# Kernel optimization log

Measured on AMD Instinct MI355X. Metric: run time of the kernel, lower is better.

Reference implementation:

```python
import jax, jax.numpy as jnp
import numpy as np

FFT_NORM = "forward"


def _deq_cplx(qp, scale, mn):
    # qp stores (q_int8 + 127) in [0, 254]; dequant: qp*scale + min, last dim = (re, im)
    f = qp.astype(jnp.float32) * scale + mn
    return jax.lax.complex(f[..., 0], f[..., 1])


def setup_inputs() -> dict:
    key = jax.random.key(0)
    ks = jax.random.split(key, 16)
    B, Cin, Cout, H, W = 8, 32, 32, 256, 256
    NxW, NyW = 32, 17            # half-modes of the spectral weight
    r0, r1, r2, r3 = 16, 16, 16, 9  # Tucker ranks
    inp = {
        "x": jax.random.normal(ks[0], (B, Cin, H, W), dtype=jnp.float32),
        "core_scale": jax.random.uniform(ks[1], (), jnp.float32, 0.001, 0.02),
        "core_min": jax.random.normal(ks[2], (), jnp.float32) * 0.1,
        "factor_scales": jax.random.uniform(ks[3], (4,), jnp.float32, 0.001, 0.02),
        "factor_mins": jax.random.normal(ks[4], (4,), jnp.float32) * 0.1,
        "b_scale": jax.random.uniform(ks[5], (), jnp.float32, 0.001, 0.02),
        "b_min": jax.random.normal(ks[6], (), jnp.float32) * 0.1,
        "q_core": jax.random.randint(ks[7], (r0, r1, r2, r3, 2), 0, 255, jnp.int32),
        "q_f0": jax.random.randint(ks[8], (Cin, r0, 2), 0, 255, jnp.int32),
        "q_f1": jax.random.randint(ks[9], (Cout, r1, 2), 0, 255, jnp.int32),
        "q_f2": jax.random.randint(ks[10], (NxW, r2, 2), 0, 255, jnp.int32),
        "q_f3": jax.random.randint(ks[11], (NyW, r3, 2), 0, 255, jnp.int32),
        "q_bias": jax.random.randint(ks[12], (Cout,), 0, 255, jnp.int32),
    }
    return inp


def reference(x, core_scale, core_min, factor_scales, factor_mins, b_scale, b_min,
              q_core, q_f0, q_f1, q_f2, q_f3, q_bias):
    # 1) rFFT over the last two (spatial) dims
    x_fft = jnp.fft.rfftn(x, axes=(-2, -1), norm=FFT_NORM)  # [B, Cin, Nx, Ny_r] c64

    # 2) dequantize Tucker core + factors, reconstruct complex weight via multi_mode_dot
    core = _deq_cplx(q_core, core_scale, core_min)                       # [r0,r1,r2,r3]
    F0 = _deq_cplx(q_f0, factor_scales[0], factor_mins[0])               # [Cin, r0]
    F1 = _deq_cplx(q_f1, factor_scales[1], factor_mins[1])               # [Cout, r1]
    F2 = _deq_cplx(q_f2, factor_scales[2], factor_mins[2])               # [NxW, r2]
    F3 = _deq_cplx(q_f3, factor_scales[3], factor_mins[3])               # [NyW, r3]
    W = jnp.einsum('ijkl,ai,bj,ck,dl->abcd', core, F0, F1, F2, F3)       # [Cin,Cout,NxW,NyW]

    B, Cin, Nx, Ny_r = x_fft.shape
    CinW, Cout, NxW, NyW = W.shape
    assert Cin == CinW

    # 3) centered-slice channel mixing (faithful to the original double loop)
    cx, nx_neg, nx_pos = Nx // 2, NxW // 2, NxW // 2 + NxW % 2
    cy, ny_neg, ny_pos = Ny_r // 2, NyW // 2, NyW // 2 + NyW % 2
    sx = slice(cx - nx_neg, cx + nx_pos)
    sy = slice(cy - ny_neg, cy + ny_pos)
    Wx = slice(0, nx_pos + nx_neg)
    Wy = slice(0, ny_pos + ny_neg)

    mixed = jnp.einsum('bixy,ioxy->boxy', x_fft[:, :, sx, sy], W[:, :, Wx, Wy])
    out_fft = jnp.zeros((B, Cout, Nx, Ny_r), dtype=x_fft.dtype).at[:, :, sx, sy].set(mixed)

    # 4) inverse rFFT back to the original spatial size
    x_out = jnp.fft.irfftn(out_fft, s=x.shape[2:], axes=(-2, -1), norm=FFT_NORM)

    # 5) dequantized bias (real)
    bias = q_bias.astype(jnp.float32) * b_scale + b_min
    return x_out + bias[None, :, None, None]
```

## Files before the change

### kernel.cpp

```cpp
#include <hip/hip_runtime.h>


__device__ __forceinline__ float2 cfma(float2 a, float2 b, float2 c) {
    c.x = fmaf(a.x, b.x, fmaf(-a.y, b.y, c.x));
    c.y = fmaf(a.x, b.y, fmaf(a.y, b.x, c.y));
    return c;
}
__device__ __forceinline__ float2 cmul(float2 a, float2 b) {
    return make_float2(a.x*b.x - a.y*b.y, a.x*b.y + a.y*b.x);
}

__global__ __launch_bounds__(256) void wprep_kernel(
    const int* __restrict__ q_core, const int* __restrict__ q_f3,
    const float* __restrict__ core_scale, const float* __restrict__ core_min,
    const float* __restrict__ f_scales, const float* __restrict__ f_mins,
    float2* __restrict__ CL)
{
    int d = blockIdx.x >> 4, k = blockIdx.x & 15;
    int ij = threadIdx.x;
    float cs = *core_scale, cm = *core_min;
    float s3 = f_scales[3], m3 = f_mins[3];
    const int* qc = q_core + ((ij*16 + k)*9)*2;
    float2 acc = make_float2(0.f, 0.f);
#pragma unroll
    for (int l = 0; l < 9; ++l) {
        int2 q = *(const int2*)(qc + l*2);
        float2 ce = make_float2(q.x*cs + cm, q.y*cs + cm);
        float2 f3 = make_float2(q_f3[(d*9+l)*2]*s3 + m3, q_f3[(d*9+l)*2+1]*s3 + m3);
        acc = cfma(ce, f3, acc);
    }
    CL[(d*16 + k)*256 + ij] = acc;
}

__global__ __launch_bounds__(256) void weights_kernel(
    const float2* __restrict__ CL, const int* __restrict__ q_f0,
    const int* __restrict__ q_f1, const int* __restrict__ q_f2,
    const float* __restrict__ f_scales, const float* __restrict__ f_mins,
    float2* __restrict__ W4)
{
    __shared__ float2 F0s[512], F1s[512];
    __shared__ float2 C2p[16*17];
    __shared__ float2 A2p[16*33];
    int t = threadIdx.x, m = blockIdx.x;
    int c = m / 17, d = m % 17;
    float s0 = f_scales[0], m0 = f_mins[0];
    float s1 = f_scales[1], m1 = f_mins[1];
    float s2 = f_scales[2], m2 = f_mins[2];

    for (int e = t; e < 512; e += 256) {
        F0s[e] = make_float2(q_f0[2*e]*s0 + m0, q_f0[2*e+1]*s0 + m0);
        F1s[e] = make_float2(q_f1[2*e]*s1 + m1, q_f1[2*e+1]*s1 + m1);
    }
    {
        float2 acc = make_float2(0.f, 0.f);
#pragma unroll
        for (int k = 0; k < 16; ++k) {
            float2 clv = CL[(d*16 + k)*256 + t];
            float2 f2 = make_float2(q_f2[(c*16+k)*2]*s2 + m2,
                                    q_f2[(c*16+k)*2+1]*s2 + m2);
            acc = cfma(clv, f2, acc);
        }
        __syncthreads();
        C2p[(t >> 4)*17 + (t & 15)] = acc;
    }
    __syncthreads();
#pragma unroll
    for (int r = 0; r < 2; ++r) {
        int e = t + r*256; int i = e & 15, b = e >> 4;
        float2 acc = make_float2(0.f, 0.f);
#pragma unroll
        for (int j = 0; j < 16; ++j)
            acc = cfma(C2p[i*17 + j], F1s[b*16 + j], acc);
        A2p[i*33 + b] = acc;
    }
    __syncthreads();
    {
        int b = t & 31, a0 = t >> 5;
#pragma unroll
        for (int q = 0; q < 4; ++q) {
            int a = a0 + 8*q;
            float2 acc = make_float2(0.f, 0.f);
#pragma unroll
            for (int i = 0; i < 16; ++i)
                acc = cfma(F0s[a*16 + i], A2p[i*33 + b], acc);
            W4[m*1024 + a*32 + b] = acc;
        }
    }
}

template<int P>
__device__ __forceinline__ void quad_acc(float& ar, float& ai, float xv, float tx, float ty) {
    if (P == 0) { ar = fmaf(xv, tx, ar);  ai = fmaf(xv, ty, ai); }
    if (P == 1) { ar = fmaf(xv, ty, ar);  ai = fmaf(-xv, tx, ai); }
    if (P == 2) { ar = fmaf(-xv, tx, ar); ai = fmaf(-xv, ty, ai); }
    if (P == 3) { ar = fmaf(-xv, ty, ar); ai = fmaf(xv, tx, ai); }
}

template<int KY0, int NKY>
__device__ __forceinline__ void fwdw_body(int lane, int row0, const float* xs,
                                          float2* __restrict__ A1)
{
    float ar[NKY], ai[NKY], tr[NKY], ti[NKY], sr[NKY], si[NKY];
#pragma unroll
    for (int j = 0; j < NKY; ++j) {
        ar[j] = 0.f; ai[j] = 0.f;
        const int kk = KY0 + j + 56;
        float a = kk * (1.f/128.f);
        sr[j] = cospif(a); si[j] = -sinpif(a);
        tr[j] = 1.f; ti[j] = 0.f;
    }
    for (int w = 0; w < 64; ++w) {
        float xv0 = xs[w*65 + lane];
        float xv1 = xs[(w+64)*65 + lane];
        float xv2 = xs[(w+128)*65 + lane];
        float xv3 = xs[(w+192)*65 + lane];
#pragma unroll
        for (int j = 0; j < NKY; ++j) {
            float tx = tr[j], ty = ti[j];
            const int pj = (KY0 + 56 + j) & 3;
            switch (pj) {
                case 0:
                    quad_acc<0>(ar[j], ai[j], xv0, tx, ty);
                    quad_acc<0>(ar[j], ai[j], xv1, tx, ty);
                    quad_acc<0>(ar[j], ai[j], xv2, tx, ty);
                    quad_acc<0>(ar[j], ai[j], xv3, tx, ty);
                    break;
                case 1:
                    quad_acc<0>(ar[j], ai[j], xv0, tx, ty);
                    quad_acc<1>(ar[j], ai[j], xv1, tx, ty);
                    quad_acc<2>(ar[j], ai[j], xv2, tx, ty);
                    quad_acc<3>(ar[j], ai[j], xv3, tx, ty);
                    break;
                case 2:
                    quad_acc<0>(ar[j], ai[j], xv0, tx, ty);
                    quad_acc<2>(ar[j], ai[j], xv1, tx, ty);
                    quad_acc<0>(ar[j], ai[j], xv2, tx, ty);
                    quad_acc<2>(ar[j], ai[j], xv3, tx, ty);
                    break;
                default:
                    quad_acc<0>(ar[j], ai[j], xv0, tx, ty);
                    quad_acc<3>(ar[j], ai[j], xv1, tx, ty);
                    quad_acc<2>(ar[j], ai[j], xv2, tx, ty);
                    quad_acc<1>(ar[j], ai[j], xv3, tx, ty);
                    break;
            }
            tr[j] = fmaf(tx, sr[j], -ty*si[j]);
            ti[j] = fmaf(tx, si[j],  ty*sr[j]);
        }
    }
    int row = row0 + lane;
#pragma unroll
    for (int j = 0; j < NKY; ++j)
        A1[(KY0 + j)*65536 + row] = make_float2(ar[j], ai[j]);
}

__global__ __launch_bounds__(256) void fwd_w_kernel(const float* __restrict__ x,
                                                    float2* __restrict__ A1)
{
    __shared__ float xs[256*65];
    int tid = threadIdx.x;
    int row0 = blockIdx.x * 64;
    const float2* xf2 = (const float2*)x;
    for (int i2 = tid; i2 < 8192; i2 += 256) {
        int r = i2 >> 7, w2 = i2 & 127;
        float2 v = xf2[(size_t)(row0 + r)*128 + w2];
        xs[(2*w2)*65 + r]   = v.x;
        xs[(2*w2+1)*65 + r] = v.y;
    }
    __syncthreads();
    int lane = tid & 63, g = tid >> 6;
    if      (g == 0) fwdw_body<0, 5>(lane, row0, xs, A1);
    else if (g == 1) fwdw_body<5, 4>(lane, row0, xs, A1);
    else if (g == 2) fwdw_body<9, 4>(lane, row0, xs, A1);
    else             fwdw_body<13,4>(lane, row0, xs, A1);
}

__global__ __launch_bounds__(256) void fwd_h_kernel(const float2* __restrict__ A1,
                                                    float2* __restrict__ X)
{
    __shared__ float2 tbl[256];
    __shared__ float as_re[8*264];
    __shared__ float as_im[8*264];
    int tid = threadIdx.x;
    int ky = blockIdx.x >> 5, bi0 = (blockIdx.x & 31) * 8;
    tbl[tid] = make_float2(cospif(tid * (1.f/128.f)), -sinpif(tid * (1.f/128.f)));
    for (int idx = tid; idx < 2048; idx += 256) {
        int b = idx >> 8, h = idx & 255;
        float2 v = A1[ky*65536 + (bi0 + b)*256 + h];
        int ad = (h >> 5)*264 + (h & 31)*8 + b;
        as_re[ad] = v.x; as_im[ad] = v.y;
    }
    __syncthreads();
    int lane = tid & 63, g = tid >> 6;
    int bl = lane & 7, q = lane >> 3;
    int kx0 = g * 8;
    float2 acc[8];
#pragma unroll
    for (int j = 0; j < 8; ++j) acc[j] = make_float2(0.f, 0.f);
    int base = q*264 + bl;
    for (int hh = 0; hh < 32; ++hh) {
        float ar = as_re[base + hh*8];
        float ai = as_im[base + hh*8];
#pragma unroll
        for (int j = 0; j < 8; ++j) {
            int kk = kx0 + j + 112;
            float2 t = tbl[(kk * hh) & 255];
            acc[j].x = fmaf(ar, t.x, fmaf(-ai, t.y, acc[j].x));
            acc[j].y = fmaf(ar, t.y, fmaf( ai, t.x, acc[j].y));
        }
    }
    float2 fstep = tbl[q * 32];
    float2 f = make_float2(1.f, 0.f);
#pragma unroll
    for (int j = 0; j < 8; ++j) {
        float2 v = cmul(acc[j], f);
        v.x += __shfl_xor(v.x, 8);  v.y += __shfl_xor(v.y, 8);
        v.x += __shfl_xor(v.x, 16); v.y += __shfl_xor(v.y, 16);
        v.x += __shfl_xor(v.x, 32); v.y += __shfl_xor(v.y, 32);
        acc[j] = v;
        f = cmul(f, fstep);
    }
    if (q == 0) {
        const float inv = 1.f / 65536.f;
#pragma unroll
        for (int j = 0; j < 8; ++j)
            X[((kx0 + j)*17 + ky)*256 + bi0 + bl] =
                make_float2(acc[j].x * inv, acc[j].y * inv);
    }
}

__global__ __launch_bounds__(256) void mix_kernel(const float2* __restrict__ X,
                                                  const float2* __restrict__ W4,
                                                  float2* __restrict__ Mx)
{
    __shared__ float2 Xs[256];
    __shared__ float2 Ws[1024];
    int tid = threadIdx.x, mode = blockIdx.x;
    Xs[tid] = X[mode*256 + tid];
    for (int idx = tid; idx < 1024; idx += 256) Ws[idx] = W4[mode*1024 + idx];
    __syncthreads();
    int b = tid >> 5, o = tid & 31;
    float2 acc = make_float2(0.f, 0.f);
#pragma unroll
    for (int i = 0; i < 32; ++i)
        acc = cfma(Xs[b*32 + i], Ws[i*32 + o], acc);
    Mx[mode*256 + tid] = acc;
}

template<int KY0, int NK>
__device__ __forceinline__ void invh_part(int h, int hh, const float2* ms, float2* Ts)
{
    float2 acc[NK];
#pragma unroll
    for (int j = 0; j < NK; ++j) acc[j] = make_float2(0.f, 0.f);
    int n0 = (112 * h) & 255;
    float tr = cospif(n0 * (1.f/128.f)), ti = sinpif(n0 * (1.f/128.f));
    float sr = cospif(h  * (1.f/128.f)), si = sinpif(h  * (1.f/128.f));
    for (int kx = 0; kx < 32; ++kx) {
#pragma unroll
        for (int j = 0; j < NK; ++j) {
            float2 mv = ms[kx*17 + KY0 + j];
            acc[j].x = fmaf(mv.x, tr, fmaf(-mv.y, ti, acc[j].x));
            acc[j].y = fmaf(mv.x, ti, fmaf( mv.y, tr, acc[j].y));
        }
        float ntr = fmaf(tr, sr, -ti*si);
        ti = fmaf(tr, si, ti*sr);
        tr = ntr;
    }
#pragma unroll
    for (int j = 0; j < NK; ++j) Ts[hh*18 + KY0 + j] = acc[j];
}

__global__ __launch_bounds__(256) void inv_kernel(const float2* __restrict__ Mx,
                                                  const int* __restrict__ q_bias,
                                                  const float* __restrict__ b_scale,
                                                  const float* __restrict__ b_min,
                                                  float* __restrict__ out)
{
    __shared__ float2 ms[544];
    __shared__ __align__(16) float2 Ts[32*18];
    int tid = threadIdx.x;
    int bo = blockIdx.x & 255, hc = blockIdx.x >> 8;
    for (int idx = tid; idx < 544; idx += 256) ms[idx] = Mx[idx*256 + bo];
    __syncthreads();
    {
        int hh = tid & 31, g = tid >> 5;
        int h = hc*32 + hh;
        if (g < 7) {
            switch (g) {
                case 0: invh_part<0, 2>(h, hh, ms, Ts); break;
                case 1: invh_part<2, 2>(h, hh, ms, Ts); break;
                case 2: invh_part<4, 2>(h, hh, ms, Ts); break;
                case 3: invh_part<6, 2>(h, hh, ms, Ts); break;
                case 4: invh_part<8, 2>(h, hh, ms, Ts); break;
                case 5: invh_part<10,2>(h, hh, ms, Ts); break;
                default:invh_part<12,2>(h, hh, ms, Ts); break;
            }
        } else {
            invh_part<14,3>(h, hh, ms, Ts);
        }
    }
    __syncthreads();
    {
        int w0 = tid & 63, hs = tid >> 6;
        float C[17], S[17];
        {
            int n0 = (56 * w0) & 255;
            float tr = cospif(n0 * (1.f/128.f)), ti = sinpif(n0 * (1.f/128.f));
            float sr = cospif(w0 * (1.f/128.f)), si = sinpif(w0 * (1.f/128.f));
#pragma unroll
            for (int ky = 0; ky < 17; ++ky) {
                C[ky] = tr; S[ky] = ti;
                float ntr = fmaf(tr, sr, -ti*si);
                ti = fmaf(tr, si, ti*sr);
                tr = ntr;
            }
        }
        float bias = q_bias[bo & 31] * (*b_scale) + (*b_min);
        float* obase = out + (size_t)bo*65536 + (size_t)hc*32*256;

#pragma unroll
        for (int r = 0; r < 8; ++r) {
            int hh = hs*8 + r;
            const float4* tp = (const float4*)&Ts[hh*18];
            float R0 = 0.f, R1 = 0.f, R2 = 0.f, R3 = 0.f, I1 = 0.f, I3 = 0.f;
#pragma unroll
            for (int kp = 0; kp < 9; ++kp) {
                float vx0, vy0, vx1 = 0.f, vy1 = 0.f;
                if (kp < 8) {
                    float4 v4 = tp[kp];
                    vx0 = v4.x; vy0 = v4.y; vx1 = v4.z; vy1 = v4.w;
                } else {
                    float2 v2 = Ts[hh*18 + 16];
                    vx0 = v2.x; vy0 = v2.y;
                }
#pragma unroll
                for (int half = 0; half < 2; ++half) {
                    if (kp == 8 && half == 1) break;
                    const int ky = 2*kp + half;
                    float vx = half ? vx1 : vx0;
                    float vy = half ? vy1 : vy0;
                    float ur = fmaf(vx, C[ky], -vy*S[ky]);
                    if ((ky & 1) == 0) {
                        if ((ky & 3) == 0) R0 += ur; else R2 += ur;
                    } else {
                        float ui = fmaf(vx, S[ky], vy*C[ky]);
                        if ((ky & 3) == 1) { R1 += ur; I1 += ui; }
                        else               { R3 += ur; I3 += ui; }
                    }
                }
            }
            float e02 = R0 + R2, d02 = R0 - R2;
            float e13 = R1 + R3, di  = I3 - I1;
            float q0 = e02 + e13, q2 = e02 - e13;
            float q1 = d02 + di,  q3 = d02 - di;
            obase[hh*256 + w0]       = fmaf(2.f, q0, bias);
            obase[hh*256 + w0 + 64]  = fmaf(2.f, q1, bias);
            obase[hh*256 + w0 + 128] = fmaf(2.f, q2, bias);
            obase[hh*256 + w0 + 192] = fmaf(2.f, q3, bias);
        }
    }
}

extern "C" void kernel_launch(void* const* d_in, const int* in_sizes, int n_in,
                              void* d_out, int out_size, void* d_ws, size_t ws_size,
                              hipStream_t stream) {
    const float* x          = (const float*)d_in[0];
    const float* core_scale = (const float*)d_in[1];
    const float* core_min   = (const float*)d_in[2];
    const float* f_scales   = (const float*)d_in[3];
    const float* f_mins     = (const float*)d_in[4];
    const float* b_scale    = (const float*)d_in[5];
    const float* b_min      = (const float*)d_in[6];
    const int* q_core = (const int*)d_in[7];
    const int* q_f0   = (const int*)d_in[8];
    const int* q_f1   = (const int*)d_in[9];
    const int* q_f2   = (const int*)d_in[10];
    const int* q_f3   = (const int*)d_in[11];
    const int* q_bias = (const int*)d_in[12];
    float* out = (float*)d_out;

    float2* ws = (float2*)d_ws;
    float2* A1 = ws;
    float2* W4 = ws + 1114112;
    float2* X  = W4 + 557056;
    float2* Mx = X + 139264;
    float2* CL = Mx + 139264;
    (void)ws_size; (void)n_in; (void)in_sizes; (void)out_size;

    wprep_kernel<<<272, 256, 0, stream>>>(q_core, q_f3, core_scale, core_min,
                                          f_scales, f_mins, CL);
    weights_kernel<<<544, 256, 0, stream>>>(CL, q_f0, q_f1, q_f2,
                                            f_scales, f_mins, W4);
    fwd_w_kernel<<<1024, 256, 0, stream>>>(x, A1);
    fwd_h_kernel<<<544, 256, 0, stream>>>(A1, X);
    mix_kernel<<<544, 256, 0, stream>>>(X, W4, Mx);
    inv_kernel<<<2048, 256, 0, stream>>>(Mx, q_bias, b_scale, b_min, out);
}
```

Measured before the change: 199.8 us.

## Split width DFT by frequency residue mod 4 with precomputed twiddle table

The width-direction partial DFT now folds the four quarter-length input segments with butterflies at load time (sums and differences), so each frequency class (k mod 4 = 0, 1, 2, 3) is computed from 64 combined samples instead of 256. The twiddles come from a shared-memory table indexed by (k*w) mod 256 rather than being advanced by a recurrence. This cuts the inner-loop FMA count roughly in half and removes drift from the twiddle recurrence. In exchange it adds shared-memory table reads and puts a different per-group workload on each wave (group 0 handles 5 frequencies, the others handle 4).

```diff
diff --git a/kernel.cpp b/kernel.cpp
--- a/kernel.cpp
+++ b/kernel.cpp
@@ -88,91 +88,90 @@
     }
 }
 
-template<int P>
-__device__ __forceinline__ void quad_acc(float& ar, float& ai, float xv, float tx, float ty) {
-    if (P == 0) { ar = fmaf(xv, tx, ar);  ai = fmaf(xv, ty, ai); }
-    if (P == 1) { ar = fmaf(xv, ty, ar);  ai = fmaf(-xv, tx, ai); }
-    if (P == 2) { ar = fmaf(-xv, tx, ar); ai = fmaf(-xv, ty, ai); }
-    if (P == 3) { ar = fmaf(-xv, ty, ar); ai = fmaf(xv, tx, ai); }
-}
-
-template<int KY0, int NKY>
-__device__ __forceinline__ void fwdw_body(int lane, int row0, const float* xs,
-                                          float2* __restrict__ A1)
-{
-    float ar[NKY], ai[NKY], tr[NKY], ti[NKY], sr[NKY], si[NKY];
-#pragma unroll
-    for (int j = 0; j < NKY; ++j) {
-        ar[j] = 0.f; ai[j] = 0.f;
-        const int kk = KY0 + j + 56;
-        float a = kk * (1.f/128.f);
-        sr[j] = cospif(a); si[j] = -sinpif(a);
-        tr[j] = 1.f; ti[j] = 0.f;
-    }
-    for (int w = 0; w < 64; ++w) {
-        float xv0 = xs[w*65 + lane];
-        float xv1 = xs[(w+64)*65 + lane];
-        float xv2 = xs[(w+128)*65 + lane];
-        float xv3 = xs[(w+192)*65 + lane];
-#pragma unroll
-        for (int j = 0; j < NKY; ++j) {
-            float tx = tr[j], ty = ti[j];
-            const int pj = (KY0 + 56 + j) & 3;
-            switch (pj) {
-                case 0:
-                    quad_acc<0>(ar[j], ai[j], xv0, tx, ty);
-                    quad_acc<0>(ar[j], ai[j], xv1, tx, ty);
-                    quad_acc<0>(ar[j], ai[j], xv2, tx, ty);
-                    quad_acc<0>(ar[j], ai[j], xv3, tx, ty);
-                    break;
-                case 1:
-                    quad_acc<0>(ar[j], ai[j], xv0, tx, ty);
-                    quad_acc<1>(ar[j], ai[j], xv1, tx, ty);
-                    quad_acc<2>(ar[j], ai[j], xv2, tx, ty);
-                    quad_acc<3>(ar[j], ai[j], xv3, tx, ty);
-                    break;
-                case 2:
-                    quad_acc<0>(ar[j], ai[j], xv0, tx, ty);
-                    quad_acc<2>(ar[j], ai[j], xv1, tx, ty);
-                    quad_acc<0>(ar[j], ai[j], xv2, tx, ty);
-                    quad_acc<2>(ar[j], ai[j], xv3, tx, ty);
-                    break;
-                default:
-                    quad_acc<0>(ar[j], ai[j], xv0, tx, ty);
-                    quad_acc<3>(ar[j], ai[j], xv1, tx, ty);
-                    quad_acc<2>(ar[j], ai[j], xv2, tx, ty);
-                    quad_acc<1>(ar[j], ai[j], xv3, tx, ty);
-                    break;
-            }
-            tr[j] = fmaf(tx, sr[j], -ty*si[j]);
-            ti[j] = fmaf(tx, si[j],  ty*sr[j]);
-        }
-    }
-    int row = row0 + lane;
-#pragma unroll
-    for (int j = 0; j < NKY; ++j)
-        A1[(KY0 + j)*65536 + row] = make_float2(ar[j], ai[j]);
-}
-
 __global__ __launch_bounds__(256) void fwd_w_kernel(const float* __restrict__ x,
                                                     float2* __restrict__ A1)
 {
-    __shared__ float xs[256*65];
+    __shared__ float ys0[64*65], ys2[64*65], yd02[64*65], yd13[64*65];
+    __shared__ float2 twl[17*64];
     int tid = threadIdx.x;
     int row0 = blockIdx.x * 64;
+
+    for (int i = tid; i < 17*64; i += 256) {
+        int ki = i >> 6, wp = i & 63;
+        int n = ((56 + ki) * wp) & 255;
+        float a = n * (1.f/128.f);
+        twl[i] = make_float2(cospif(a), -sinpif(a));
+    }
     const float2* xf2 = (const float2*)x;
-    for (int i2 = tid; i2 < 8192; i2 += 256) {
-        int r = i2 >> 7, w2 = i2 & 127;
-        float2 v = xf2[(size_t)(row0 + r)*128 + w2];
-        xs[(2*w2)*65 + r]   = v.x;
-        xs[(2*w2+1)*65 + r] = v.y;
-    }
-    __syncthreads();
+    for (int i2 = tid; i2 < 2048; i2 += 256) {
+        int r = i2 >> 5, w2 = i2 & 31;
+        const float2* xb = xf2 + (size_t)(row0 + r) * 128 + w2;
+        float2 a0 = xb[0], a1 = xb[32], a2 = xb[64], a3 = xb[96];
+        int ad = (2*w2)*65 + r;
+        float s02 = a0.x + a2.x, s13 = a1.x + a3.x;
+        ys0[ad] = s02 + s13;  ys2[ad] = s02 - s13;
+        yd02[ad] = a0.x - a2.x;  yd13[ad] = a1.x - a3.x;
+        s02 = a0.y + a2.y;  s13 = a1.y + a3.y;
+        ys0[ad+65] = s02 + s13;  ys2[ad+65] = s02 - s13;
+        yd02[ad+65] = a0.y - a2.y;  yd13[ad+65] = a1.y - a3.y;
+    }
+    __syncthreads();
+
     int lane = tid & 63, g = tid >> 6;
-    if      (g == 0) fwdw_body<0, 5>(lane, row0, xs, A1);
-    else if (g == 1) fwdw_body<5, 4>(lane, row0, xs, A1);
-    else if (g == 2) fwdw_body<9, 4>(lane, row0, xs, A1);
-    else             fwdw_body<13,4>(lane, row0, xs, A1);
+    int row = row0 + lane;
+    if (g == 0) {
+        float2 acc[5] = {};
+        for (int wp = 0; wp < 64; ++wp) {
+            float y = ys0[wp*65 + lane];
+#pragma unroll
+            for (int j = 0; j < 5; ++j) {
+                float2 t = twl[(4*j)*64 + wp];
+                acc[j].x = fmaf(y, t.x, acc[j].x);
+                acc[j].y = fmaf(y, t.y, acc[j].y);
+            }
+        }
+#pragma unroll
+        for (int j = 0; j < 5; ++j) A1[(4*j)*65536 + row] = acc[j];
+    } else if (g == 2) {
+        float2 acc[4] = {};
+        for (int wp = 0; wp < 64; ++wp) {
+            float y = ys2[wp*65 + lane];
+#pragma unroll
+            for (int j = 0; j < 4; ++j) {
+                float2 t = twl[(2+4*j)*64 + wp];
+                acc[j].x = fmaf(y, t.x, acc[j].x);
+                acc[j].y = fmaf(y, t.y, acc[j].y);
+            }
+        }
+#pragma unroll
+        for (int j = 0; j < 4; ++j) A1[(2+4*j)*65536 + row] = acc[j];
+    } else if (g == 1) {
+        float2 acc[4] = {};
+        for (int wp = 0; wp < 64; ++wp) {
+            float a = yd02[wp*65 + lane], b = yd13[wp*65 + lane];
+#pragma unroll
+            for (int j = 0; j < 4; ++j) {
+                float2 t = twl[(1+4*j)*64 + wp];
+                acc[j].x = fmaf(t.x, a, fmaf( t.y, b, acc[j].x));
+                acc[j].y = fmaf(t.y, a, fmaf(-t.x, b, acc[j].y));
+            }
+        }
+#pragma unroll
+        for (int j = 0; j < 4; ++j) A1[(1+4*j)*65536 + row] = acc[j];
+    } else {
+        float2 acc[4] = {};
+        for (int wp = 0; wp < 64; ++wp) {
+            float a = yd02[wp*65 + lane], b = yd13[wp*65 + lane];
+#pragma unroll
+            for (int j = 0; j < 4; ++j) {
+                float2 t = twl[(3+4*j)*64 + wp];
+                acc[j].x = fmaf(t.x, a, fmaf(-t.y, b, acc[j].x));
+                acc[j].y = fmaf(t.y, a, fmaf( t.x, b, acc[j].y));
+            }
+        }
+#pragma unroll
+        for (int j = 0; j < 4; ++j) A1[(3+4*j)*65536 + row] = acc[j];
+    }
 }
 
 __global__ __launch_bounds__(256) void fwd_h_kernel(const float2* __restrict__ A1,
```

Result: no change. 196.0 us (-1.9%).
